# Kernel tuning notes

Hardware: AMD Instinct MI355X
Metric: run time of the kernel (lower is better)

## Reference

```python
import jax, jax.numpy as jnp
import numpy as np

N = 50000      # nodes
E = 800000     # edges (avg degree 16)
D = 64         # emb_dim
L = 5          # num_layer
BN_EPS = 1e-5


def setup_inputs() -> dict:
    key = jax.random.key(0)
    ks = jax.random.split(key, 10)
    x = jax.random.randint(ks[0], (N,), 0, 1)                      # indices into 1-row embedding
    edge_index = jax.random.randint(ks[1], (2, E), 0, N)
    edge_attr = jax.random.normal(ks[2], (E, 7), dtype=jnp.float32)
    s = lambda k, shape: (jax.random.normal(k, shape, dtype=jnp.float32) * 0.05)
    node_emb = s(ks[3], (1, D))
    # per-layer GINConv params, stacked on a leading layer axis for lax.scan
    We = s(ks[4], (L, 7, D));   be = jnp.zeros((L, D), jnp.float32)      # edge_encoder
    eps = jnp.zeros((L,), jnp.float32)                                   # GIN eps
    W1 = s(ks[5], (L, D, 2 * D)); b1 = jnp.zeros((L, 2 * D), jnp.float32)  # mlp linear1
    g1 = jnp.ones((L, 2 * D), jnp.float32); bb1 = jnp.zeros((L, 2 * D), jnp.float32)  # mlp BN
    W2 = s(ks[6], (L, 2 * D, D)); b2 = jnp.zeros((L, D), jnp.float32)    # mlp linear2
    g2 = jnp.ones((L, D), jnp.float32); bb2 = jnp.zeros((L, D), jnp.float32)  # outer BN
    return dict(x=x, edge_index=edge_index, edge_attr=edge_attr, node_emb=node_emb,
                We=We, be=be, eps=eps, W1=W1, b1=b1, g1=g1, bb1=bb1,
                W2=W2, b2=b2, g2=g2, bb2=bb2)


def _bn(a, g, b):
    # BatchNorm1d in training mode: batch statistics over node axis, biased var
    m = a.mean(axis=0)
    v = jnp.var(a, axis=0)
    return (a - m) * jax.lax.rsqrt(v + BN_EPS) * g + b


def reference(x, edge_index, edge_attr, node_emb, We, be, eps,
              W1, b1, g1, bb1, W2, b2, g2, bb2):
    src, dst = edge_index[0], edge_index[1]
    h = node_emb[x]                                    # [N, D]
    relu_flags = jnp.arange(L) < (L - 1)               # ReLU on all but last layer

    def step(h, p):
        We_, be_, eps_, W1_, b1_, g1_, bb1_, W2_, b2_, g2_, bb2_, flag = p
        ee = edge_attr @ We_ + be_                     # [E, D] edge embeddings
        msg = jax.nn.relu(h[src] + ee)                 # gather + elementwise
        agg = jax.ops.segment_sum(msg, dst, num_segments=N)  # scatter-add
        z = (1.0 + eps_) * h + agg                     # GIN combine
        a = jax.nn.relu(_bn(z @ W1_ + b1_, g1_, bb1_)) # mlp: lin -> BN -> ReLU
        hb = _bn(a @ W2_ + b2_, g2_, bb2_)             # lin -> outer BN
        h_new = jnp.where(flag, jax.nn.relu(hb), hb)   # dropout omitted (eval)
        return h_new, None

    h, _ = jax.lax.scan(step, h, (We, be, eps, W1, b1, g1, bb1, W2, b2, g2, bb2, relu_flags))
    return h                                           # JK='last'
```

## Files before the change

### kernel.cpp

```cpp
#include <hip/hip_runtime.h>
#include <hip/hip_fp16.h>

#define NN 50000
#define EE 800000
#define NB 782

typedef _Float16 f16x8 __attribute__((ext_vector_type(8)));
typedef _Float16 f16x4 __attribute__((ext_vector_type(4)));
typedef _Float16 f16x2 __attribute__((ext_vector_type(2)));
typedef float f32x4 __attribute__((ext_vector_type(4)));

__device__ __forceinline__ unsigned h2u(__half2 h) {
    union { __half2 h; unsigned u; } c; c.h = h; return c.u;
}
__device__ __forceinline__ f16x2 u2h(unsigned u) {
    union { unsigned u; f16x2 h; } c; c.u = u; return c.h;
}

__global__ __launch_bounds__(256) void hist_kernel(const int* __restrict__ ei,
                                                   int* __restrict__ deg) {
    const int e = (blockIdx.x << 8) + threadIdx.x;
    atomicAdd(&deg[ei[EE + e]], 1);
}

__global__ __launch_bounds__(256) void scanA_kernel(const int* __restrict__ deg,
                                                    int* __restrict__ bsum) {
    __shared__ int sm[256];
    const int t = threadIdx.x;
    const int i = (blockIdx.x << 8) + t;
    sm[t] = (i < NN) ? ((deg[i] + 7) & ~7) : 0;
    __syncthreads();
    for (int o = 128; o > 0; o >>= 1) {
        if (t < o) sm[t] += sm[t + o];
        __syncthreads();
    }
    if (t == 0) bsum[blockIdx.x] = sm[0];
}

__global__ __launch_bounds__(256) void scanB_kernel(int* __restrict__ bsum) {
    __shared__ int sm[256];
    const int t = threadIdx.x;
    const int v = (t < 196) ? bsum[t] : 0;
    sm[t] = v;
    __syncthreads();
    for (int o = 1; o < 256; o <<= 1) {
        const int u = (t >= o) ? sm[t - o] : 0;
        __syncthreads();
        sm[t] += u;
        __syncthreads();
    }
    bsum[t] = sm[t] - v;
}

__global__ __launch_bounds__(256) void scanC_kernel(const int* __restrict__ deg,
                                                    const int* __restrict__ bsum,
                                                    int* __restrict__ off,
                                                    int* __restrict__ cur) {
    __shared__ int sm[256];
    const int t = threadIdx.x;
    const int i = (blockIdx.x << 8) + t;
    const int v = (i < NN) ? ((deg[i] + 7) & ~7) : 0;
    sm[t] = v;
    __syncthreads();
    for (int o = 1; o < 256; o <<= 1) {
        const int u = (t >= o) ? sm[t - o] : 0;
        __syncthreads();
        sm[t] += u;
        __syncthreads();
    }
    const int excl = bsum[blockIdx.x] + sm[t] - v;
    if (i < NN) { off[i] = excl; cur[i] = excl; }
    else if (i == NN) off[NN] = excl;
}

__global__ __launch_bounds__(256) void scatter_kernel(const int* __restrict__ ei,
                                                      const float* __restrict__ ea,
                                                      int* __restrict__ cur,
                                                      int4* __restrict__ pea) {
    const int e = (blockIdx.x << 8) + threadIdx.x;
    const int src = ei[e];
    const int dst = ei[EE + e];
    const float* a = ea + e * 7;
    const unsigned h0 = __half_as_ushort(__float2half(a[0]));
    const unsigned h1 = __half_as_ushort(__float2half(a[1]));
    const unsigned h2 = __half_as_ushort(__float2half(a[2]));
    const unsigned h3 = __half_as_ushort(__float2half(a[3]));
    const unsigned h4 = __half_as_ushort(__float2half(a[4]));
    const unsigned h5 = __half_as_ushort(__float2half(a[5]));
    const unsigned h6 = __half_as_ushort(__float2half(a[6]));
    const int pos = atomicAdd(&cur[dst], 1);
    pea[pos] = make_int4((int)(h0 | (h1 << 16)), (int)(h2 | (h3 << 16)),
                         (int)(h4 | (h5 << 16)), (int)(h6 | ((unsigned)src << 16)));
}

__global__ __launch_bounds__(256) void fill_kernel(
    const int* __restrict__ off, const int* __restrict__ cur,
    int4* __restrict__ pea, unsigned* __restrict__ h32)
{
    const int i = (blockIdx.x << 8) + threadIdx.x;
    if (i < 32) h32[(NN << 5) + i] = 0xFBFFFBFFu;
    if (i >= NN * 8) return;
    const int n = i >> 3, j = i & 7;
    const int pos = cur[n] + j;
    if (pos < off[n + 1])
        pea[pos] = make_int4(0, 0, 0, (int)(((unsigned)NN) << 16));
}

__global__ __launch_bounds__(256) void bnstats_kernel(
    const float* __restrict__ part, const int nb, const int half,
    const float* __restrict__ g, const float* __restrict__ bb,
    float* __restrict__ scsh)
{
    __shared__ float ss[256], qq[256];
    const int c = blockIdx.x, t = threadIdx.x;
    const int stride = half << 1;
    float s = 0.f, q = 0.f;
    for (int b = t; b < nb; b += 256) {
        s += part[b * stride + c];
        q += part[b * stride + half + c];
    }
    ss[t] = s; qq[t] = q;
    __syncthreads();
    for (int o = 128; o > 0; o >>= 1) {
        if (t < o) { ss[t] += ss[t + o]; qq[t] += qq[t + o]; }
        __syncthreads();
    }
    if (t == 0) {
        const float m = ss[0] * (1.0f / NN);
        const float v = fmaxf(qq[0] * (1.0f / NN) - m * m, 0.0f);
        const float sc = g[c] * rsqrtf(v + 1e-5f);
        scsh[c] = sc;
        scsh[half + c] = bb[c] - m * sc;
    }
}

__global__ __launch_bounds__(256) void wprep_kernel(
    const float* __restrict__ W1, const float* __restrict__ W2,
    const float* __restrict__ We, const float* __restrict__ be,
    _Float16* __restrict__ W1s, _Float16* __restrict__ W2s,
    unsigned* __restrict__ Wepk, unsigned* __restrict__ be2)
{
    const int i = (blockIdx.x << 8) + threadIdx.x;
    if (i < 40960) {
        const int l = i >> 13, j = i & 8191, k = j >> 7, n = j & 127;
        W1s[(l << 13) + ((((k >> 3) << 7) + n) << 3) + (k & 7)] = (_Float16)W1[i];
    } else if (i < 81920) {
        const int i2 = i - 40960;
        const int l = i2 >> 13, j = i2 & 8191, k = j >> 6, n = j & 63;
        W2s[(l << 13) + ((((k >> 3) << 6) + n) << 3) + (k & 7)] = (_Float16)W2[i2];
    } else if (i < 83040) {
        const int i3 = i - 81920;
        const int l = i3 / 224;
        const int r = i3 - l * 224;
        const int k = r >> 5, s = r & 31;
        const float* W = We + l * 448 + (k << 6) + (s << 1);
        Wepk[i3] = h2u(__floats2half2_rn(W[0], W[1]));
    } else if (i < 83200) {
        const int i4 = i - 83040;
        const int l = i4 >> 5, s = i4 & 31;
        const float* B = be + (l << 6) + (s << 1);
        be2[i4] = h2u(__floats2half2_rn(B[0], B[1]));
    }
}

__global__ __launch_bounds__(256) void hprep_kernel(
    const float* __restrict__ y2, const float* __restrict__ scsh2,
    __half* __restrict__ h16)
{
    const int i4 = (blockIdx.x << 8) + threadIdx.x;
    const float4 v = ((const float4*)y2)[i4];
    const int d0 = (i4 << 2) & 63;
    const float a = fmaxf(fmaf(v.x, scsh2[d0 + 0], scsh2[64 + d0 + 0]), 0.f);
    const float b = fmaxf(fmaf(v.y, scsh2[d0 + 1], scsh2[64 + d0 + 1]), 0.f);
    const float c = fmaxf(fmaf(v.z, scsh2[d0 + 2], scsh2[64 + d0 + 2]), 0.f);
    const float d = fmaxf(fmaf(v.w, scsh2[d0 + 3], scsh2[64 + d0 + 3]), 0.f);
    *(int2*)(h16 + (i4 << 2)) =
        make_int2((int)h2u(__floats2half2_rn(a, b)),
                  (int)h2u(__floats2half2_rn(c, d)));
}

__global__ __launch_bounds__(256) void hprep0_kernel(
    const int* __restrict__ x, const float* __restrict__ nemb,
    __half* __restrict__ h16)
{
    const int i4 = (blockIdx.x << 8) + threadIdx.x;
    const int n = i4 >> 4;
    const float4 v = ((const float4*)nemb)[(x[n] << 4) + (i4 & 15)];
    *(int2*)(h16 + (i4 << 2)) =
        make_int2((int)h2u(__floats2half2_rn(v.x, v.y)),
                  (int)h2u(__floats2half2_rn(v.z, v.w)));
}

__global__ __launch_bounds__(256) void gather_kernel(
    const int* __restrict__ off, const int4* __restrict__ pea,
    const unsigned* __restrict__ h32,
    const unsigned* __restrict__ Wepk, const unsigned* __restrict__ be2,
    const float* __restrict__ epsp,
    unsigned* __restrict__ z32)
{
    const int t = threadIdx.x;
    const int lane = t & 63;
    const int s = lane & 31;
    const int n = (blockIdx.x << 3) + ((t >> 6) << 1) + (lane >> 5);

    const f16x2 w0 = u2h(Wepk[s]),       w1 = u2h(Wepk[32 + s]),
                w2 = u2h(Wepk[64 + s]),  w3 = u2h(Wepk[96 + s]),
                w4 = u2h(Wepk[128 + s]), w5 = u2h(Wepk[160 + s]),
                w6 = u2h(Wepk[192 + s]);
    const f16x2 beh = u2h(be2[s]);

    const int e0 = off[n], e1 = off[n + 1];

    f16x2 acc2 = (f16x2){(_Float16)0.f, (_Float16)0.f};
    for (int e = e0; e < e1; e += 8) {
        int4 pk[8];
#pragma unroll
        for (int j = 0; j < 8; ++j) pk[j] = pea[e + j];
        unsigned hv[8];
#pragma unroll
        for (int j = 0; j < 8; ++j) {
            const int src = (int)(((unsigned)pk[j].w) >> 16);
            hv[j] = h32[(src << 5) + s];
        }
#pragma unroll
        for (int j = 0; j < 8; ++j) {
            const f16x2 a01 = u2h((unsigned)pk[j].x);
            const f16x2 a23 = u2h((unsigned)pk[j].y);
            const f16x2 a45 = u2h((unsigned)pk[j].z);
            const f16x2 a6x = u2h((unsigned)pk[j].w);
            f16x2 ee = beh;
            ee += (f16x2){a01[0], a01[0]} * w0;
            ee += (f16x2){a01[1], a01[1]} * w1;
            ee += (f16x2){a23[0], a23[0]} * w2;
            ee += (f16x2){a23[1], a23[1]} * w3;
            ee += (f16x2){a45[0], a45[0]} * w4;
            ee += (f16x2){a45[1], a45[1]} * w5;
            ee += (f16x2){a6x[0], a6x[0]} * w6;
            f16x2 m2 = u2h(hv[j]) + ee;
            const _Float16 zz = (_Float16)0.f;
            m2 = (f16x2){ m2[0] > zz ? m2[0] : zz, m2[1] > zz ? m2[1] : zz };
            acc2 += m2;
        }
    }
    const f16x2 hn2 = u2h(h32[(n << 5) + s]);
    const float e1f = 1.0f + epsp[0];
    const float zLo = fmaf(e1f, (float)hn2[0], (float)acc2[0]);
    const float zHi = fmaf(e1f, (float)hn2[1], (float)acc2[1]);
    z32[(n << 5) + s] = h2u(__floats2half2_rn(zLo, zHi));
}

__global__ __launch_bounds__(256) void mm1_kernel(
    const _Float16* __restrict__ z16, const _Float16* __restrict__ W1s,
    const float* __restrict__ b1p, _Float16* __restrict__ y1h,
    float* __restrict__ part1)
{
    __shared__ float smS[4][128], smQ[4][128];
    const int t = threadIdx.x;
    const int wv = t >> 6, lane = t & 63;
    const int q = lane >> 4, ln = lane & 15;
    const int r0 = blockIdx.x << 6;

    const int rowm = r0 + (wv << 4) + ln;
    const f16x8 af0 = *(const f16x8*)(z16 + rowm * 64 + (q << 3));
    const f16x8 af1 = *(const f16x8*)(z16 + rowm * 64 + 32 + (q << 3));

    f32x4 acc[8];
#pragma unroll
    for (int n0 = 0; n0 < 8; ++n0) acc[n0] = (f32x4){0.f, 0.f, 0.f, 0.f};
#pragma unroll
    for (int n0 = 0; n0 < 8; ++n0) {
        const f16x8 bf0 = *(const f16x8*)(W1s + (((q << 7) + (n0 << 4) + ln) << 3));
        const f16x8 bf1 = *(const f16x8*)(W1s + ((((4 + q) << 7) + (n0 << 4) + ln) << 3));
        acc[n0] = __builtin_amdgcn_mfma_f32_16x16x32_f16(af0, bf0, acc[n0], 0, 0, 0);
        acc[n0] = __builtin_amdgcn_mfma_f32_16x16x32_f16(af1, bf1, acc[n0], 0, 0, 0);
    }

    const int baseRow = r0 + (wv << 4) + (q << 2);
#pragma unroll
    for (int n0 = 0; n0 < 8; ++n0) {
        const int col = (n0 << 4) + ln;
        const float bb = b1p[col];
        float s = 0.f, sq = 0.f;
#pragma unroll
        for (int rg = 0; rg < 4; ++rg) {
            const int row = baseRow + rg;
            const float y = acc[n0][rg] + bb;
            y1h[row * 128 + col] = (_Float16)y;
            const float m = (row < NN) ? 1.f : 0.f;
            s = fmaf(m, y, s); sq = fmaf(m, y * y, sq);
        }
        s += __shfl_xor(s, 16); s += __shfl_xor(s, 32);
        sq += __shfl_xor(sq, 16); sq += __shfl_xor(sq, 32);
        if (lane < 16) { smS[wv][col] = s; smQ[wv][col] = sq; }
    }
    __syncthreads();
    if (t < 128) {
        const float s = smS[0][t] + smS[1][t] + smS[2][t] + smS[3][t];
        const float q2 = smQ[0][t] + smQ[1][t] + smQ[2][t] + smQ[3][t];
        part1[(blockIdx.x << 8) + t] = s;
        part1[(blockIdx.x << 8) + 128 + t] = q2;
    }
}

__global__ __launch_bounds__(256) void mm2_kernel(
    const _Float16* __restrict__ y1h, const float* __restrict__ scsh1,
    const _Float16* __restrict__ W2s, const float* __restrict__ b2,
    float* __restrict__ y2, float* __restrict__ part2)
{
    __shared__ float smS[4][64], smQ[4][64];
    const int t = threadIdx.x;
    const int wv = t >> 6, lane = t & 63;
    const int q = lane >> 4, ln = lane & 15;
    const int r0 = blockIdx.x << 6;

    const int rowm = r0 + (wv << 4) + ln;
    f16x8 af[4];
#pragma unroll
    for (int ks = 0; ks < 4; ++ks) {
        const int k0 = (ks << 5) + (q << 3);
        const f16x8 raw = *(const f16x8*)(y1h + rowm * 128 + k0);
        const float4 scA = *(const float4*)(scsh1 + k0);
        const float4 scB = *(const float4*)(scsh1 + k0 + 4);
        const float4 shA = *(const float4*)(scsh1 + 128 + k0);
        const float4 shB = *(const float4*)(scsh1 + 128 + k0 + 4);
        const float sc[8] = {scA.x, scA.y, scA.z, scA.w, scB.x, scB.y, scB.z, scB.w};
        const float sh[8] = {shA.x, shA.y, shA.z, shA.w, shB.x, shB.y, shB.z, shB.w};
        f16x8 a;
#pragma unroll
        for (int j = 0; j < 8; ++j)
            a[j] = (_Float16)fmaxf(fmaf((float)raw[j], sc[j], sh[j]), 0.f);
        af[ks] = a;
    }

    f32x4 acc[4];
#pragma unroll
    for (int n0 = 0; n0 < 4; ++n0) acc[n0] = (f32x4){0.f, 0.f, 0.f, 0.f};
#pragma unroll
    for (int n0 = 0; n0 < 4; ++n0) {
#pragma unroll
        for (int ks = 0; ks < 4; ++ks) {
            const f16x8 bf = *(const f16x8*)(
                W2s + (((((ks << 2) + q) << 6) + (n0 << 4) + ln) << 3));
            acc[n0] = __builtin_amdgcn_mfma_f32_16x16x32_f16(af[ks], bf, acc[n0], 0, 0, 0);
        }
    }

    const int baseRow = r0 + (wv << 4) + (q << 2);
#pragma unroll
    for (int n0 = 0; n0 < 4; ++n0) {
        const int col = (n0 << 4) + ln;
        const float bb = b2[col];
        float s = 0.f, sq = 0.f;
#pragma unroll
        for (int rg = 0; rg < 4; ++rg) {
            const int row = baseRow + rg;
            const float y = acc[n0][rg] + bb;
            y2[row * 64 + col] = y;
            const float m = (row < NN) ? 1.f : 0.f;
            s = fmaf(m, y, s); sq = fmaf(m, y * y, sq);
        }
        s += __shfl_xor(s, 16); s += __shfl_xor(s, 32);
        sq += __shfl_xor(sq, 16); sq += __shfl_xor(sq, 32);
        if (lane < 16) { smS[wv][col] = s; smQ[wv][col] = sq; }
    }
    __syncthreads();
    if (t < 64) {
        const float s = smS[0][t] + smS[1][t] + smS[2][t] + smS[3][t];
        const float q2 = smQ[0][t] + smQ[1][t] + smQ[2][t] + smQ[3][t];
        part2[(blockIdx.x << 7) + t] = s;
        part2[(blockIdx.x << 7) + 64 + t] = q2;
    }
}

__global__ __launch_bounds__(256) void final_kernel(
    const float* __restrict__ y2, const float* __restrict__ scsh2,
    float* __restrict__ out)
{
    const int i = (blockIdx.x << 8) + threadIdx.x;
    if (i >= NN * 64) return;
    const int d = i & 63;
    out[i] = fmaf(y2[i], scsh2[d], scsh2[64 + d]);
}

extern "C" void kernel_launch(void* const* d_in, const int* in_sizes, int n_in,
                              void* d_out, int out_size, void* d_ws, size_t ws_size,
                              hipStream_t stream)
{
    const int*   x    = (const int*)d_in[0];
    const int*   ei   = (const int*)d_in[1];
    const float* ea   = (const float*)d_in[2];
    const float* nemb = (const float*)d_in[3];
    const float* We   = (const float*)d_in[4];
    const float* be   = (const float*)d_in[5];
    const float* eps  = (const float*)d_in[6];
    const float* W1   = (const float*)d_in[7];
    const float* b1   = (const float*)d_in[8];
    const float* g1   = (const float*)d_in[9];
    const float* bb1  = (const float*)d_in[10];
    const float* W2   = (const float*)d_in[11];
    const float* b2   = (const float*)d_in[12];
    const float* g2   = (const float*)d_in[13];
    const float* bb2  = (const float*)d_in[14];
    float* out = (float*)d_out;

    int*      iws   = (int*)d_ws;
    float*    fws   = (float*)d_ws;
    int*      off   = iws + 0;
    int*      deg   = iws + 50048;
    int*      cur   = iws + 100096;
    int*      bsum  = iws + 150144;
    float*    scsh1 = fws + 150400;
    float*    scsh2 = fws + 150656;
    float*    part1 = fws + 150784;
    float*    part2 = fws + 350976;
    _Float16* W1s   = (_Float16*)(fws + 451072);
    _Float16* W2s   = (_Float16*)(fws + 471552);
    unsigned* Wepk  = (unsigned*)(fws + 492032);
    unsigned* be2   = (unsigned*)(fws + 493152);
    int4*     pea   = (int4*)(iws + 493312);
    _Float16* z16   = (_Float16*)(fws + 5093312);
    _Float16* y1h   = (_Float16*)(fws + 6694848);
    float*    y2    = fws + 6694848;
    __half*   h16   = (__half*)(fws + 9897920);

    hipMemsetAsync(deg, 0, 50000 * sizeof(int), stream);

    hist_kernel   <<<3125, 256, 0, stream>>>(ei, deg);
    scanA_kernel  <<<196,  256, 0, stream>>>(deg, bsum);
    scanB_kernel  <<<1,    256, 0, stream>>>(bsum);
    scanC_kernel  <<<196,  256, 0, stream>>>(deg, bsum, off, cur);
    scatter_kernel<<<3125, 256, 0, stream>>>(ei, ea, cur, pea);
    fill_kernel   <<<1563, 256, 0, stream>>>(off, cur, pea, (unsigned*)h16);
    wprep_kernel  <<<325,  256, 0, stream>>>(W1, W2, We, be, W1s, W2s, Wepk, be2);
    hprep0_kernel <<<3125, 256, 0, stream>>>(x, nemb, h16);

    for (int l = 0; l < 5; ++l) {
        gather_kernel<<<6250, 256, 0, stream>>>(
            off, pea, (const unsigned*)h16, Wepk + l * 224, be2 + l * 32,
            eps + l, (unsigned*)z16);

        mm1_kernel<<<NB, 256, 0, stream>>>(z16, W1s + l * 8192, b1 + l * 128,
                                           y1h, part1);

        bnstats_kernel<<<128, 256, 0, stream>>>(part1, NB, 128,
                                                g1 + l * 128, bb1 + l * 128, scsh1);

        mm2_kernel<<<NB, 256, 0, stream>>>(y1h, scsh1, W2s + l * 8192, b2 + l * 64,
                                           y2, part2);

        bnstats_kernel<<<64, 256, 0, stream>>>(part2, NB, 64,
                                               g2 + l * 64, bb2 + l * 64, scsh2);

        if (l < 4)
            hprep_kernel<<<3125, 256, 0, stream>>>(y2, scsh2, h16);
    }

    final_kernel<<<12500, 256, 0, stream>>>(y2, scsh2, out);
}
```

Measured before the change: 489.3 us.

## Replace global-atomic CSR build with two-pass bucketed binning via shared-memory atomics

```diff
diff --git a/kernel.cpp b/kernel.cpp
--- a/kernel.cpp
+++ b/kernel.cpp
@@ -4,6 +4,8 @@
 #define NN 50000
 #define EE 800000
 #define NB 782
+#define NBKT 196
+#define BCAP 5120
 
 typedef _Float16 f16x8 __attribute__((ext_vector_type(8)));
 typedef _Float16 f16x4 __attribute__((ext_vector_type(4)));
@@ -17,10 +19,66 @@
     union { unsigned u; f16x2 h; } c; c.u = u; return c.h;
 }
 
-__global__ __launch_bounds__(256) void hist_kernel(const int* __restrict__ ei,
-                                                   int* __restrict__ deg) {
-    const int e = (blockIdx.x << 8) + threadIdx.x;
-    atomicAdd(&deg[ei[EE + e]], 1);
+__global__ __launch_bounds__(256) void bin_kernel(
+    const int* __restrict__ ei, const float* __restrict__ ea,
+    int* __restrict__ bktcur, int4* __restrict__ srec,
+    unsigned short* __restrict__ sdst)
+{
+    __shared__ int cnt[NBKT], base[NBKT];
+    const int t = threadIdx.x;
+    if (t < NBKT) cnt[t] = 0;
+    __syncthreads();
+    const int e0 = blockIdx.x << 10;
+    int bkk[4], rk[4], loc[4];
+#pragma unroll
+    for (int j = 0; j < 4; ++j) {
+        const int e = e0 + (j << 8) + t;
+        if (e < EE) {
+            const int d = ei[EE + e];
+            bkk[j] = d >> 8;
+            loc[j] = d & 255;
+            rk[j] = atomicAdd(&cnt[bkk[j]], 1);
+        } else bkk[j] = -1;
+    }
+    __syncthreads();
+    if (t < NBKT) base[t] = cnt[t] ? atomicAdd(&bktcur[t], cnt[t]) : 0;
+    __syncthreads();
+#pragma unroll
+    for (int j = 0; j < 4; ++j) {
+        if (bkk[j] < 0) continue;
+        const int slot = base[bkk[j]] + rk[j];
+        if (slot >= BCAP) continue;
+        const int pos = bkk[j] * BCAP + slot;
+        const int e = e0 + (j << 8) + t;
+        const int src = ei[e];
+        const float* a = ea + e * 7;
+        const unsigned h0 = __half_as_ushort(__float2half(a[0]));
+        const unsigned h1 = __half_as_ushort(__float2half(a[1]));
+        const unsigned h2 = __half_as_ushort(__float2half(a[2]));
+        const unsigned h3 = __half_as_ushort(__float2half(a[3]));
+        const unsigned h4 = __half_as_ushort(__float2half(a[4]));
+        const unsigned h5 = __half_as_ushort(__float2half(a[5]));
+        const unsigned h6 = __half_as_ushort(__float2half(a[6]));
+        srec[pos] = make_int4((int)(h0 | (h1 << 16)), (int)(h2 | (h3 << 16)),
+                              (int)(h4 | (h5 << 16)), (int)(h6 | ((unsigned)src << 16)));
+        sdst[pos] = (unsigned short)loc[j];
+    }
+}
+
+__global__ __launch_bounds__(256) void bcount2_kernel(
+    const int* __restrict__ bktcur, const unsigned short* __restrict__ sdst,
+    int* __restrict__ deg)
+{
+    __shared__ int nc[256];
+    const int b = blockIdx.x, t = threadIdx.x;
+    nc[t] = 0;
+    __syncthreads();
+    const int nEdge = bktcur[b];
+    const int sbase = b * BCAP;
+    for (int i = t; i < nEdge; i += 256) atomicAdd(&nc[(int)sdst[sbase + i]], 1);
+    __syncthreads();
+    const int node = (b << 8) + t;
+    if (node < NN) deg[node] = nc[t];
 }
 
 __global__ __launch_bounds__(256) void scanA_kernel(const int* __restrict__ deg,
@@ -73,37 +131,29 @@
     else if (i == NN) off[NN] = excl;
 }
 
-__global__ __launch_bounds__(256) void scatter_kernel(const int* __restrict__ ei,
-                                                      const float* __restrict__ ea,
-                                                      int* __restrict__ cur,
-                                                      int4* __restrict__ pea) {
-    const int e = (blockIdx.x << 8) + threadIdx.x;
-    const int src = ei[e];
-    const int dst = ei[EE + e];
-    const float* a = ea + e * 7;
-    const unsigned h0 = __half_as_ushort(__float2half(a[0]));
-    const unsigned h1 = __half_as_ushort(__float2half(a[1]));
-    const unsigned h2 = __half_as_ushort(__float2half(a[2]));
-    const unsigned h3 = __half_as_ushort(__float2half(a[3]));
-    const unsigned h4 = __half_as_ushort(__float2half(a[4]));
-    const unsigned h5 = __half_as_ushort(__float2half(a[5]));
-    const unsigned h6 = __half_as_ushort(__float2half(a[6]));
-    const int pos = atomicAdd(&cur[dst], 1);
-    pea[pos] = make_int4((int)(h0 | (h1 << 16)), (int)(h2 | (h3 << 16)),
-                         (int)(h4 | (h5 << 16)), (int)(h6 | ((unsigned)src << 16)));
-}
-
-__global__ __launch_bounds__(256) void fill_kernel(
-    const int* __restrict__ off, const int* __restrict__ cur,
-    int4* __restrict__ pea, unsigned* __restrict__ h32)
-{
-    const int i = (blockIdx.x << 8) + threadIdx.x;
-    if (i < 32) h32[(NN << 5) + i] = 0xFBFFFBFFu;
-    if (i >= NN * 8) return;
-    const int n = i >> 3, j = i & 7;
-    const int pos = cur[n] + j;
-    if (pos < off[n + 1])
-        pea[pos] = make_int4(0, 0, 0, (int)(((unsigned)NN) << 16));
+__global__ __launch_bounds__(256) void place2_kernel(
+    const int* __restrict__ bktcur, const int* __restrict__ off,
+    const int4* __restrict__ srec, const unsigned short* __restrict__ sdst,
+    int4* __restrict__ pea)
+{
+    __shared__ int curs[256];
+    const int b = blockIdx.x, t = threadIdx.x;
+    const int node = (b << 8) + t;
+    curs[t] = (node < NN) ? off[node] : 0;
+    __syncthreads();
+    const int nEdge = bktcur[b];
+    const int sbase = b * BCAP;
+    for (int i = t; i < nEdge; i += 256) {
+        const int ln = (int)sdst[sbase + i];
+        const int p = atomicAdd(&curs[ln], 1);
+        pea[p] = srec[sbase + i];
+    }
+    __syncthreads();
+    if (node < NN) {
+        const int end = off[node + 1];
+        for (int p = curs[t]; p < end; ++p)
+            pea[p] = make_int4(0, 0, 0, (int)(((unsigned)NN) << 16));
+    }
 }
 
 __global__ __launch_bounds__(256) void bnstats_kernel(
@@ -181,9 +231,12 @@
 
 __global__ __launch_bounds__(256) void hprep0_kernel(
     const int* __restrict__ x, const float* __restrict__ nemb,
-    __half* __restrict__ h16)
+    __half* __restrict__ h16, unsigned* __restrict__ z32)
 {
     const int i4 = (blockIdx.x << 8) + threadIdx.x;
+    if (blockIdx.x == 0 && threadIdx.x < 32)
+        ((unsigned*)h16)[(NN << 5) + threadIdx.x] = 0xFBFFFBFFu;
+    if (i4 < 1536) z32[1600000 + i4] = 0u;
     const int n = i4 >> 4;
     const float4 v = ((const float4*)nemb)[(x[n] << 4) + (i4 & 15)];
     *(int2*)(h16 + (i4 << 2)) =
@@ -423,16 +476,20 @@
     float*    y2    = fws + 6694848;
     __half*   h16   = (__half*)(fws + 9897920);
 
-    hipMemsetAsync(deg, 0, 50000 * sizeof(int), stream);
-
-    hist_kernel   <<<3125, 256, 0, stream>>>(ei, deg);
+    int4*           srec   = (int4*)(fws + 5093312);
+    unsigned short* sdst   = (unsigned short*)(fws + 9107392);
+    int*            bktcur = iws + 150784;
+
+    hipMemsetAsync(bktcur, 0, NBKT * sizeof(int), stream);
+
+    bin_kernel    <<<782,  256, 0, stream>>>(ei, ea, bktcur, srec, sdst);
+    bcount2_kernel<<<NBKT, 256, 0, stream>>>(bktcur, sdst, deg);
     scanA_kernel  <<<196,  256, 0, stream>>>(deg, bsum);
     scanB_kernel  <<<1,    256, 0, stream>>>(bsum);
     scanC_kernel  <<<196,  256, 0, stream>>>(deg, bsum, off, cur);
-    scatter_kernel<<<3125, 256, 0, stream>>>(ei, ea, cur, pea);
-    fill_kernel   <<<1563, 256, 0, stream>>>(off, cur, pea, (unsigned*)h16);
+    place2_kernel <<<NBKT, 256, 0, stream>>>(bktcur, off, srec, sdst, pea);
     wprep_kernel  <<<325,  256, 0, stream>>>(W1, W2, We, be, W1s, W2s, Wepk, be2);
-    hprep0_kernel <<<3125, 256, 0, stream>>>(x, nemb, h16);
+    hprep0_kernel <<<3125, 256, 0, stream>>>(x, nemb, h16, (unsigned*)z16);
 
     for (int l = 0; l < 5; ++l) {
         gather_kernel<<<6250, 256, 0, stream>>>(
```

Result: faster. 453.8 us (-7.3%).
